# Performance work log

Hardware: AMD Instinct MI355X
Metric: run time of the kernel (lower is better)

The kernel has to match this reference:

```python
import jax, jax.numpy as jnp
import numpy as np

COMMITMENT_COST = 0.25

def setup_inputs() -> dict:
    key = jax.random.key(0)
    k1, k2 = jax.random.split(key)
    z = jax.random.normal(k1, (32768, 512), dtype=jnp.float32)
    # codebook initialized uniform(-1/K, 1/K) as in the torch module
    K = 8192
    W = jax.random.uniform(k2, (K, 512), dtype=jnp.float32, minval=-1.0 / K, maxval=1.0 / K)
    return {"z": z, "W": W}

def reference(z, W):
    # z: [B, D], W: [K, D]
    # squared-distance expansion: ||z||^2 + ||w||^2 - 2 z.w
    d2 = (jnp.sum(z * z, axis=1, keepdims=True)
          + jnp.sum(W * W, axis=1)
          - 2.0 * jnp.einsum('bd,kd->bk', z, W))  # [B, K]
    indices = jnp.argmin(d2, axis=1)              # [B]
    z_q_raw = W[indices]                          # [B, D]
    e_latent_loss = jnp.mean((jax.lax.stop_gradient(z_q_raw) - z) ** 2)
    q_latent_loss = jnp.mean((z_q_raw - jax.lax.stop_gradient(z)) ** 2)
    vq_loss = q_latent_loss + COMMITMENT_COST * e_latent_loss
    # straight-through estimator
    z_q = z + jax.lax.stop_gradient(z_q_raw - z)
    return (z_q, indices, vq_loss)
```

## Files before the change

kernel.cpp:

```cpp
#include <hip/hip_runtime.h>
#include <stdint.h>


#define B_ROWS 32768
#define DIM    512
#define KCODES 8192
#define SUPERS 2
#define TILES  32

typedef short bhalf8_t __attribute__((ext_vector_type(8)));
typedef float f32x4_t  __attribute__((ext_vector_type(4)));

__device__ __forceinline__ float b2f(unsigned short u) {
    return __uint_as_float(((unsigned int)u) << 16);
}
__device__ __forceinline__ unsigned short f2b(float f) {
    unsigned int x = __float_as_uint(f);
    return (unsigned short)((x + 0x7FFFu + ((x >> 16) & 1u)) >> 16);
}
__device__ __forceinline__ void gl_lds16(const void* g, void* l) {
    __builtin_amdgcn_global_load_lds(
        (const __attribute__((address_space(1))) unsigned int*)g,
        (__attribute__((address_space(3))) unsigned int*)l, 16, 0, 0);
}

__global__ __launch_bounds__(256) void k_split(const float4* __restrict__ src,
                                               ushort4* __restrict__ dst, int n4) {
    int i = blockIdx.x * 256 + threadIdx.x;
    int stride = gridDim.x * 256;
    for (; i < n4; i += stride) {
        float4 v = src[i];
        ushort4 h;
        h.x = f2b(v.x); h.y = f2b(v.y); h.z = f2b(v.z); h.w = f2b(v.w);
        dst[i] = h;
    }
}

__global__ __launch_bounds__(256) void k_pairsq(const float* __restrict__ X,
                                                float* __restrict__ out, int nrows) {
    int wid = threadIdx.x >> 6, lane = threadIdx.x & 63;
    int r = blockIdx.x * 4 + wid;
    if (r >= nrows) return;
    int b = lane >> 3, j = lane & 7;
    float acc = 0.f;
    if (b < 4) {
        const float* x = X + (size_t)r * DIM + b * 128 + j;
        float v = x[0];
        acc = __fmul_rn(v, v);
        for (int i = 1; i < 16; i++) {
            float w = x[8 * i];
            acc = __fadd_rn(acc, __fmul_rn(w, w));
        }
    }
    float t = __fadd_rn(acc, __shfl_xor(acc, 1));
    t = __fadd_rn(t, __shfl_xor(t, 2));
    t = __fadd_rn(t, __shfl_xor(t, 4));
    float u = __fadd_rn(t, __shfl_xor(t, 8));
    u = __fadd_rn(u, __shfl_xor(u, 16));
    if (lane == 0) out[r] = u;
}

__global__ __launch_bounds__(256) void k_argmin(const unsigned short* __restrict__ Zh,
                                                const unsigned short* __restrict__ Wh,
                                                const float* __restrict__ ww,
                                                float2* __restrict__ part) {
    __shared__ alignas(16) unsigned char smem[32768];
    const int tid = threadIdx.x;
    const int lane = tid & 63, w = tid >> 6;
    const int wm = w >> 1, wn = w & 1;
    const int lane15 = lane & 15, q = lane >> 4;
    const int b = blockIdx.x;
    const int super = b & 1;
    const int rb = (b >> 1) * 128;

    uint32_t p1[4][4], p2[4][4];
#pragma unroll
    for (int i = 0; i < 4; i++)
#pragma unroll
        for (int jj = 0; jj < 4; jj++) { p1[i][jj] = 0xFFFFFFFFu; p2[i][jj] = 0xFFFFFFFFu; }

    for (int tl = 0; tl < TILES; ++tl) {
        const int nt = super * 4096 + tl * 128;
        f32x4_t acc[4][4];
#pragma unroll
        for (int i = 0; i < 4; i++)
#pragma unroll
            for (int jj = 0; jj < 4; jj++) acc[i][jj] = (f32x4_t){0.f, 0.f, 0.f, 0.f};

        for (int kb = 0; kb < DIM; kb += 32) {
            __syncthreads();
#pragma unroll
            for (int l = 0; l < 2; l++) {
                int s = l * 256 + tid;
                int row = s >> 2, seg = s & 3;
                gl_lds16(Zh + (size_t)(rb + row) * DIM + kb + seg * 8, smem +        s * 16);
                gl_lds16(Wh + (size_t)(nt + row) * DIM + kb + seg * 8, smem + 8192 + s * 16);
            }
            __syncthreads();

            bhalf8_t af[4], bf[4];
#pragma unroll
            for (int f = 0; f < 4; f++) {
                int off = (f * 16 + lane15) * 64 + q * 16;
                af[f] = *(const bhalf8_t*)(smem +        (wm * 4096 + off));
                bf[f] = *(const bhalf8_t*)(smem + 8192 + (wn * 4096 + off));
            }
#pragma unroll
            for (int fm = 0; fm < 4; fm++)
#pragma unroll
                for (int fn = 0; fn < 4; fn++)
                    acc[fm][fn] = __builtin_amdgcn_mfma_f32_16x16x32_bf16(af[fm], bf[fn], acc[fm][fn], 0, 0, 0);
        }

        float cb[4];
#pragma unroll
        for (int fn = 0; fn < 4; fn++)
            cb[fn] = ww[nt + wn * 64 + fn * 16 + lane15] + 0.5f;
#pragma unroll
        for (int fm = 0; fm < 4; fm++)
#pragma unroll
            for (int r = 0; r < 4; r++)
#pragma unroll
                for (int fn = 0; fn < 4; fn++) {
                    float sv = fmaf(-2.0f, acc[fm][fn][r], cb[fn]);
                    uint32_t pk = (__float_as_uint(sv) & 0xFFFFFF80u) | (uint32_t)(tl * 4 + fn);
                    if (pk < p1[fm][r]) { p2[fm][r] = p1[fm][r]; p1[fm][r] = pk; }
                    else if (pk < p2[fm][r]) { p2[fm][r] = pk; }
                }
    }

    __syncthreads();
    uint32_t* keys = (uint32_t*)smem;
#pragma unroll
    for (int fm = 0; fm < 4; fm++)
#pragma unroll
        for (int r = 0; r < 4; r++) {
            int row = wm * 64 + fm * 16 + q * 4 + r;
            int slice = wn * 16 + lane15;
            keys[(row * 32 + slice) * 2 + 0] = p1[fm][r];
            keys[(row * 32 + slice) * 2 + 1] = p2[fm][r];
        }
    __syncthreads();
    if (tid < 128) {
        int row = tid;
        int rglob = rb + row;
        for (int s = 0; s < 8; s++) {
            uint32_t bk = 0xFFFFFFFFu; int be = 0;
            for (int e = 0; e < 64; e++) {
                uint32_t k = keys[row * 64 + e];
                if (k < bk) { bk = k; be = e; }
            }
            int slice = be >> 1;
            int id = (int)(bk & 127u);
            int n = super * 4096 + (id >> 2) * 128 + (slice >> 4) * 64 + (id & 3) * 16 + (slice & 15);
            part[((size_t)rglob * SUPERS + super) * 8 + s] =
                make_float2(__uint_as_float(bk), __int_as_float(n));
            keys[row * 64 + be] = 0xFFFFFFFFu;
        }
    }
}

__global__ __launch_bounds__(256) void k_exact(const float* __restrict__ Zf,
                                               const float* __restrict__ Wf,
                                               const float2* __restrict__ part,
                                               const float* __restrict__ zz,
                                               const float* __restrict__ ww,
                                               float* __restrict__ outf,
                                               float* __restrict__ lossp) {
    __shared__ float wsum[4];
    int wid = threadIdx.x >> 6, lane = threadIdx.x & 63;
    int r = blockIdx.x * 4 + wid;
    int c = lane >> 2, j = lane & 3;

    float2 P = part[((size_t)r * SUPERS + (c >> 3)) * 8 + (c & 7)];
    int n = __float_as_int(P.y);
    n = min(max(n, 0), KCODES - 1);

    const float* zp = Zf + (size_t)r * DIM + j;
    const float* wp = Wf + (size_t)n * DIM + j;
    float acc = 0.f;
    for (int i = 0; i < 128; i++)
        acc = __fadd_rn(acc, __fmul_rn(zp[4 * i], wp[4 * i]));
    float t = __fadd_rn(acc, __shfl_xor(acc, 1));
    t = __fadd_rn(t, __shfl_xor(t, 2));
    float dot = __shfl(t, c * 4);

    float t1 = __fadd_rn(zz[r], ww[n]);
    float t2 = __fmul_rn(2.0f, dot);
    float d2 = __fadd_rn(t1, -t2);

    float bd = (j == 0) ? d2 : 3.4e38f;
    int   bn = (j == 0) ? n  : 0x7FFFFFFF;
#pragma unroll
    for (int off = 32; off; off >>= 1) {
        float od = __shfl_xor(bd, off);
        int   on = __shfl_xor(bn, off);
        if (od < bd || (od == bd && on < bn)) { bd = od; bn = on; }
    }
    int idx = bn;

    float4 wa = *(const float4*)(Wf + (size_t)idx * DIM + lane * 8);
    float4 wb = *(const float4*)(Wf + (size_t)idx * DIM + lane * 8 + 4);
    float4 za = *(const float4*)(Zf + (size_t)r   * DIM + lane * 8);
    float4 zb = *(const float4*)(Zf + (size_t)r   * DIM + lane * 8 + 4);
    *(float4*)(outf + (size_t)r * DIM + lane * 8)     = wa;
    *(float4*)(outf + (size_t)r * DIM + lane * 8 + 4) = wb;
    float d0 = za.x - wa.x, d1 = za.y - wa.y, dd2 = za.z - wa.z, d3 = za.w - wa.w;
    float d4 = zb.x - wb.x, d5 = zb.y - wb.y, d6 = zb.z - wb.z, d7 = zb.w - wb.w;
    float ls = d0*d0 + d1*d1 + dd2*dd2 + d3*d3 + d4*d4 + d5*d5 + d6*d6 + d7*d7;
#pragma unroll
    for (int off = 32; off; off >>= 1) ls += __shfl_xor(ls, off);
    if (lane == 0) {
        outf[(size_t)B_ROWS * DIM + r] = (float)idx;
        wsum[wid] = ls;
    }
    __syncthreads();
    if (threadIdx.x == 0) lossp[blockIdx.x] = wsum[0] + wsum[1] + wsum[2] + wsum[3];
}

__global__ __launch_bounds__(256) void k_loss(const float* __restrict__ lossp,
                                              float* __restrict__ outf) {
    __shared__ float sm[256];
    float a = 0.f;
    for (int i = threadIdx.x; i < 8192; i += 256) a += lossp[i];
    sm[threadIdx.x] = a;
    __syncthreads();
    for (int s = 128; s; s >>= 1) {
        if (threadIdx.x < s) sm[threadIdx.x] += sm[threadIdx.x + s];
        __syncthreads();
    }
    if (threadIdx.x == 0)
        outf[(size_t)B_ROWS * DIM + B_ROWS] = 1.25f * sm[0] / 16777216.0f;
}

extern "C" void kernel_launch(void* const* d_in, const int* in_sizes, int n_in,
                              void* d_out, int out_size, void* d_ws, size_t ws_size,
                              hipStream_t stream) {
    (void)in_sizes; (void)n_in; (void)out_size; (void)ws_size;
    const float* Zf = (const float*)d_in[0];
    const float* Wf = (const float*)d_in[1];
    float* outf = (float*)d_out;

    unsigned short* Zh = (unsigned short*)d_out;
    unsigned short* Wh = (unsigned short*)((char*)d_out + (32ull << 20));

    float*  ww    = (float*)d_ws;
    float*  zz    = (float*)((char*)d_ws + 32768);
    float*  lossp = (float*)((char*)d_ws + 163840);
    float2* partp = (float2*)((char*)d_ws + 196608);

    k_split<<<1024, 256, 0, stream>>>((const float4*)Zf, (ushort4*)Zh, B_ROWS * DIM / 4);
    k_split<<<512,  256, 0, stream>>>((const float4*)Wf, (ushort4*)Wh, KCODES * DIM / 4);
    k_pairsq<<<KCODES / 4, 256, 0, stream>>>(Wf, ww, KCODES);
    k_pairsq<<<B_ROWS / 4, 256, 0, stream>>>(Zf, zz, B_ROWS);
    k_argmin<<<(B_ROWS / 128) * SUPERS, 256, 0, stream>>>(Zh, Wh, ww, partp);
    k_exact<<<B_ROWS / 4, 256, 0, stream>>>(Zf, Wf, partp, zz, ww, outf, lossp);
    k_loss<<<1, 256, 0, stream>>>(lossp, outf);
}
```

Before: 765.3 us.

## Double-buffer LDS tiles with async global-to-LDS prefetch in argmin GEMM

Replaces the single-buffered load/sync/compute loop with a two-stage ping-pong LDS pipeline. The next k-slice is issued via global_load_lds while the current one is consumed, using vmcnt waits and raw barriers instead of full syncthreads. The LDS layout is reordered so each lane reads contiguous fragments, and the codebook norms (+0.5) are preloaded into LDS once per block. This targets exposed global-load latency and barrier stalls in the distance GEMM, at the cost of 48KB LDS per block, which may reduce occupancy.

```diff
diff --git a/kernel.cpp b/kernel.cpp
--- a/kernel.cpp
+++ b/kernel.cpp
@@ -7,6 +7,7 @@
 #define KCODES 8192
 #define SUPERS 2
 #define TILES  32
+#define NSTEP  512
 
 typedef short bhalf8_t __attribute__((ext_vector_type(8)));
 typedef float f32x4_t  __attribute__((ext_vector_type(4)));
@@ -60,11 +61,27 @@
     if (lane == 0) out[r] = u;
 }
 
+__device__ __forceinline__ void compute_step(const unsigned char* ba,
+                                             const unsigned char* bb,
+                                             int lane, f32x4_t acc[4][4]) {
+    bhalf8_t af[4], bf[4];
+#pragma unroll
+    for (int f = 0; f < 4; f++) {
+        af[f] = *(const bhalf8_t*)(ba + f * 1024 + lane * 16);
+        bf[f] = *(const bhalf8_t*)(bb + f * 1024 + lane * 16);
+    }
+#pragma unroll
+    for (int fm = 0; fm < 4; fm++)
+#pragma unroll
+        for (int fn = 0; fn < 4; fn++)
+            acc[fm][fn] = __builtin_amdgcn_mfma_f32_16x16x32_bf16(af[fm], bf[fn], acc[fm][fn], 0, 0, 0);
+}
+
 __global__ __launch_bounds__(256) void k_argmin(const unsigned short* __restrict__ Zh,
                                                 const unsigned short* __restrict__ Wh,
                                                 const float* __restrict__ ww,
                                                 float2* __restrict__ part) {
-    __shared__ alignas(16) unsigned char smem[32768];
+    __shared__ alignas(16) unsigned char smem[49152];
     const int tid = threadIdx.x;
     const int lane = tid & 63, w = tid >> 6;
     const int wm = w >> 1, wn = w & 1;
@@ -73,49 +90,72 @@
     const int super = b & 1;
     const int rb = (b >> 1) * 128;
 
+    const int rowO0 = ((tid >> 6) << 4) | (tid & 15);
+    const int kO0   = ((tid >> 4) & 3) << 3;
+    const int dst0  = tid * 16;
+
+#define STAGE(STEP, BUF)                                                              \
+    do {                                                                              \
+        const int _tl = (STEP) >> 4;                                                  \
+        const int _kb = ((STEP) & 15) * 32;                                           \
+        const int _nt = super * 4096 + _tl * 128;                                     \
+        unsigned char* _ba = smem + (BUF) * 16384;                                    \
+        unsigned char* _bb = _ba + 8192;                                              \
+        gl_lds16(Zh + (size_t)(rb + rowO0) * DIM + _kb + kO0, _ba + dst0);            \
+        gl_lds16(Zh + (size_t)(rb + rowO0 + 64) * DIM + _kb + kO0, _ba + 4096 + dst0);\
+        gl_lds16(Wh + (size_t)(_nt + rowO0) * DIM + _kb + kO0, _bb + dst0);           \
+        gl_lds16(Wh + (size_t)(_nt + rowO0 + 64) * DIM + _kb + kO0, _bb + 4096 + dst0);\
+    } while (0)
+
+    float* wwl = (float*)(smem + 32768);
+    {
+        const float4* srcw = (const float4*)(ww + super * 4096);
+        float4* dstw = (float4*)wwl;
+        for (int i = tid; i < 1024; i += 256) {
+            float4 v = srcw[i];
+            v.x += 0.5f; v.y += 0.5f; v.z += 0.5f; v.w += 0.5f;
+            dstw[i] = v;
+        }
+    }
+
     uint32_t p1[4][4], p2[4][4];
 #pragma unroll
     for (int i = 0; i < 4; i++)
 #pragma unroll
         for (int jj = 0; jj < 4; jj++) { p1[i][jj] = 0xFFFFFFFFu; p2[i][jj] = 0xFFFFFFFFu; }
 
+    __syncthreads();
+    STAGE(0, 0);
+
     for (int tl = 0; tl < TILES; ++tl) {
-        const int nt = super * 4096 + tl * 128;
         f32x4_t acc[4][4];
 #pragma unroll
         for (int i = 0; i < 4; i++)
 #pragma unroll
             for (int jj = 0; jj < 4; jj++) acc[i][jj] = (f32x4_t){0.f, 0.f, 0.f, 0.f};
 
-        for (int kb = 0; kb < DIM; kb += 32) {
-            __syncthreads();
-#pragma unroll
-            for (int l = 0; l < 2; l++) {
-                int s = l * 256 + tid;
-                int row = s >> 2, seg = s & 3;
-                gl_lds16(Zh + (size_t)(rb + row) * DIM + kb + seg * 8, smem +        s * 16);
-                gl_lds16(Wh + (size_t)(nt + row) * DIM + kb + seg * 8, smem + 8192 + s * 16);
+        for (int k8 = 0; k8 < 16; k8 += 2) {
+            const int st = tl * 16 + k8;
+            STAGE(st + 1, 1);
+            asm volatile("s_waitcnt vmcnt(4)" ::: "memory");
+            __builtin_amdgcn_s_barrier();
+            compute_step(smem + wm * 4096, smem + 8192 + wn * 4096, lane, acc);
+            __builtin_amdgcn_s_barrier();
+            if (st + 2 < NSTEP) {
+                STAGE(st + 2, 0);
+                asm volatile("s_waitcnt vmcnt(4)" ::: "memory");
+            } else {
+                asm volatile("s_waitcnt vmcnt(0)" ::: "memory");
             }
-            __syncthreads();
-
-            bhalf8_t af[4], bf[4];
-#pragma unroll
-            for (int f = 0; f < 4; f++) {
-                int off = (f * 16 + lane15) * 64 + q * 16;
-                af[f] = *(const bhalf8_t*)(smem +        (wm * 4096 + off));
-                bf[f] = *(const bhalf8_t*)(smem + 8192 + (wn * 4096 + off));
-            }
-#pragma unroll
-            for (int fm = 0; fm < 4; fm++)
-#pragma unroll
-                for (int fn = 0; fn < 4; fn++)
-                    acc[fm][fn] = __builtin_amdgcn_mfma_f32_16x16x32_bf16(af[fm], bf[fn], acc[fm][fn], 0, 0, 0);
+            __builtin_amdgcn_s_barrier();
+            compute_step(smem + 16384 + wm * 4096, smem + 16384 + 8192 + wn * 4096, lane, acc);
+            __builtin_amdgcn_s_barrier();
         }
 
         float cb[4];
 #pragma unroll
         for (int fn = 0; fn < 4; fn++)
-            cb[fn] = ww[nt + wn * 64 + fn * 16 + lane15] + 0.5f;
+            cb[fn] = wwl[tl * 128 + wn * 64 + fn * 16 + lane15];
 #pragma unroll
         for (int fm = 0; fm < 4; fm++)
 #pragma unroll
@@ -128,6 +168,7 @@
                     else if (pk < p2[fm][r]) { p2[fm][r] = pk; }
                 }
     }
+#undef STAGE
 
     __syncthreads();
     uint32_t* keys = (uint32_t*)smem;
```

Measured after the change: 944.3 us. 1.23x slower.
